# Kernel tuning notes

Measured on AMD Instinct MI355X. Metric: run time of the kernel, lower is better.

## Reference

```python
import jax, jax.numpy as jnp
import numpy as np

B, C, H = 64, 64, 32

def _pm_cross_pairs(ks):
    # Replicates PM_cross(2, ks): pairs (i, i+j) ordered by gap j=1..ks-1, then i.
    a, b = [], []
    for j in range(1, ks):
        for i in range(ks - j):
            a.append(i)
            b.append(i + j)
    return np.array(a, dtype=np.int32), np.array(b, dtype=np.int32)

def setup_inputs() -> dict:
    key = jax.random.key(0)
    k1, k2 = jax.random.split(key)
    ia, ib = _pm_cross_pairs(H)           # 496 pairs for H=32
    hk = ia.shape[0] + 2 * H              # 560
    x = jax.random.normal(k1, (B, C, H, H), dtype=jnp.float32)
    weight = 0.1 * jax.random.normal(k2, (C, H, hk, H), dtype=jnp.float32)
    return {"x": x, "weight": weight, "idx_a": jnp.asarray(ia), "idx_b": jnp.asarray(ib)}

def reference(x, weight, idx_a, idx_b):
    # cross-term products along last axis: [B,C,H,P]
    cross = x[..., idx_a] * x[..., idx_b]
    feat = jnp.concatenate([x, x * x, cross], axis=-1)  # [B,C,H,Hk]
    # per-(channel,row) grouped matmul
    return jnp.einsum('bcij,cijo->bcio', feat, weight)
```

## Files before the change

kernel.cpp:

```cpp
#include <hip/hip_runtime.h>

#define NB 64
#define NC 64
#define NH 32
#define HK 560
#define KPAD 576

typedef __bf16 bf16x8 __attribute__((ext_vector_type(8)));
typedef float f32x4 __attribute__((ext_vector_type(4)));

__global__ __launch_bounds__(256, 4) void hconv_kernel(
    const float* __restrict__ x, const float* __restrict__ w,
    const int* __restrict__ idx_a, const int* __restrict__ idx_b,
    float* __restrict__ out)
{
    __shared__ float s_x[NB][34];
    __shared__ __align__(16) unsigned s_lut[KPAD];
    __shared__ __align__(16) unsigned short s_wT[2][32][72];

    const int t = threadIdx.x;
    const int g = blockIdx.x;
    const int c = g >> 5, i = g & 31;

    {
        const int row = t >> 3;
        const int c4 = (t & 7) * 4;
        const float* xr = x + (((size_t)row * NC + c) * NH + i) * NH;
        const float* xr2 = xr + (size_t)32 * NC * NH * NH;
        float4 v = *(const float4*)(xr + c4);
        float4 v2 = *(const float4*)(xr2 + c4);
        s_x[row][c4] = v.x;  s_x[row][c4 + 1] = v.y;
        s_x[row][c4 + 2] = v.z; s_x[row][c4 + 3] = v.w;
        s_x[row + 32][c4] = v2.x;  s_x[row + 32][c4 + 1] = v2.y;
        s_x[row + 32][c4 + 2] = v2.z; s_x[row + 32][c4 + 3] = v2.w;
        if ((t & 7) == 0) {
            s_x[row][32] = 1.0f;      s_x[row][33] = 0.0f;
            s_x[row + 32][32] = 1.0f; s_x[row + 32][33] = 0.0f;
        }
    }

    for (int k = t; k < KPAD; k += 256) {
        unsigned pa, pb;
        if (k < 32)        { pa = (unsigned)k;        pb = 32u; }
        else if (k < 64)   { pa = (unsigned)(k - 32); pb = pa;  }
        else if (k < HK)   { pa = (unsigned)idx_a[k - 64]; pb = (unsigned)idx_b[k - 64]; }
        else               { pa = 33u; pb = 33u; }
        s_lut[k] = pa | (pb << 16);
    }

    const int wv = t >> 6;
    const int lane = t & 63;
    const int lr = lane & 15;
    const int lq = lane >> 4;
    const int row = wv * 16 + lr;
    const int wo = t & 31;
    const int wkg = t >> 5;

    const float* wbase = w + (size_t)(c * NH + i) * HK * NH;

    float pv[8];
    #pragma unroll
    for (int r = 0; r < 8; ++r)
        pv[r] = wbase[(size_t)(wkg * 8 + r) * NH + wo];
    {
        bf16x8 wv8;
        #pragma unroll
        for (int r = 0; r < 8; ++r) wv8[r] = (__bf16)pv[r];
        *(bf16x8*)&s_wT[0][wo][wkg * 8] = wv8;
    }
    __syncthreads();

    f32x4 acc0 = {0.f, 0.f, 0.f, 0.f};
    f32x4 acc1 = {0.f, 0.f, 0.f, 0.f};

    for (int ch = 0; ch < 9; ++ch) {
        const int k0 = ch * 64;
        const int buf = ch & 1;

        if (ch < 8) {
            const int kb = k0 + 64 + wkg * 8;
            #pragma unroll
            for (int r = 0; r < 8; ++r) {
                const int k = kb + r;
                pv[r] = (k < HK) ? wbase[(size_t)k * NH + wo] : 0.0f;
            }
        }

        #pragma unroll
        for (int ks = 0; ks < 2; ++ks) {
            const uint4* lp = (const uint4*)&s_lut[k0 + ks * 32 + lq * 8];
            const uint4 L0 = lp[0], L1 = lp[1];
            const unsigned pr[8] = {L0.x, L0.y, L0.z, L0.w, L1.x, L1.y, L1.z, L1.w};
            bf16x8 a;
            #pragma unroll
            for (int j = 0; j < 8; ++j) {
                const float p = s_x[row][pr[j] & 0xffffu] * s_x[row][pr[j] >> 16];
                a[j] = (__bf16)p;
            }
            bf16x8 b0 = *(const bf16x8*)&s_wT[buf][lr][ks * 32 + lq * 8];
            bf16x8 b1 = *(const bf16x8*)&s_wT[buf][16 + lr][ks * 32 + lq * 8];
            acc0 = __builtin_amdgcn_mfma_f32_16x16x32_bf16(a, b0, acc0, 0, 0, 0);
            acc1 = __builtin_amdgcn_mfma_f32_16x16x32_bf16(a, b1, acc1, 0, 0, 0);
        }

        if (ch < 8) {
            bf16x8 wv8;
            #pragma unroll
            for (int r = 0; r < 8; ++r) wv8[r] = (__bf16)pv[r];
            *(bf16x8*)&s_wT[buf ^ 1][wo][wkg * 8] = wv8;
        }
        __syncthreads();
    }

    #pragma unroll
    for (int r = 0; r < 4; ++r) {
        const int b = wv * 16 + lq * 4 + r;
        float* op = out + (((size_t)b * NC + c) * NH + i) * NH;
        op[lr] = acc0[r];
        op[16 + lr] = acc1[r];
    }
}

extern "C" void kernel_launch(void* const* d_in, const int* in_sizes, int n_in,
                              void* d_out, int out_size, void* d_ws, size_t ws_size,
                              hipStream_t stream) {
    const float* x = (const float*)d_in[0];
    const float* w = (const float*)d_in[1];
    const int* idx_a = (const int*)d_in[2];
    const int* idx_b = (const int*)d_in[3];
    float* out = (float*)d_out;
    hconv_kernel<<<dim3(NC * NH), dim3(256), 0, stream>>>(x, w, idx_a, idx_b, out);
}
```

Measured before the change: 238.8 us.

## Replace per-element gather LUT with contiguous octet descriptors over padded x rows

Regroups the K dimension into 8-wide octets whose operands are contiguous runs in x (pairs sharing a gap j), so each lane reads two contiguous 8-float spans instead of 16 indexed gathers. Descriptors encode source offsets, weight row offset and valid count, and partial octets are zero-padded, which grows K from 9 to 11 chunks of 64. The index inputs are no longer read; the pair order is hardcoded to match PM_cross. Weight loads also switch to nontemporal.

Measured after the change: 278.6 us. 16.7% more time.

```diff
diff --git a/kernel.cpp b/kernel.cpp
--- a/kernel.cpp
+++ b/kernel.cpp
@@ -4,7 +4,9 @@
 #define NC 64
 #define NH 32
 #define HK 560
-#define KPAD 576
+#define NOCT 88
+#define NCHUNK 11
+#define XSTR 50
 
 typedef __bf16 bf16x8 __attribute__((ext_vector_type(8)));
 typedef float f32x4 __attribute__((ext_vector_type(4)));
@@ -14,8 +16,8 @@
     const int* __restrict__ idx_a, const int* __restrict__ idx_b,
     float* __restrict__ out)
 {
-    __shared__ float s_x[NB][34];
-    __shared__ __align__(16) unsigned s_lut[KPAD];
+    __shared__ float s_x[NB * XSTR];
+    __shared__ unsigned s_desc[NOCT];
     __shared__ __align__(16) unsigned short s_wT[2][32][72];
 
     const int t = threadIdx.x;
@@ -23,49 +25,63 @@
     const int c = g >> 5, i = g & 31;
 
     {
-        const int row = t >> 3;
-        const int c4 = (t & 7) * 4;
-        const float* xr = x + (((size_t)row * NC + c) * NH + i) * NH;
-        const float* xr2 = xr + (size_t)32 * NC * NH * NH;
-        float4 v = *(const float4*)(xr + c4);
-        float4 v2 = *(const float4*)(xr2 + c4);
-        s_x[row][c4] = v.x;  s_x[row][c4 + 1] = v.y;
-        s_x[row][c4 + 2] = v.z; s_x[row][c4 + 3] = v.w;
-        s_x[row + 32][c4] = v2.x;  s_x[row + 32][c4 + 1] = v2.y;
-        s_x[row + 32][c4 + 2] = v2.z; s_x[row + 32][c4 + 3] = v2.w;
-        if ((t & 7) == 0) {
-            s_x[row][32] = 1.0f;      s_x[row][33] = 0.0f;
-            s_x[row + 32][32] = 1.0f; s_x[row + 32][33] = 0.0f;
+        const int xrow = t >> 2, seg = t & 3;
+        const float* xr = x + (((size_t)xrow * NC + c) * NH + i) * NH + seg * 8;
+        float4 v0 = *(const float4*)(xr);
+        float4 v1 = *(const float4*)(xr + 4);
+        float* dst = &s_x[xrow * XSTR + seg * 8];
+        dst[0] = v0.x; dst[1] = v0.y; dst[2] = v0.z; dst[3] = v0.w;
+        dst[4] = v1.x; dst[5] = v1.y; dst[6] = v1.z; dst[7] = v1.w;
+        if (seg == 0) {
+            #pragma unroll
+            for (int m = 0; m < 8; ++m) {
+                s_x[xrow * XSTR + 32 + m] = 0.0f;
+                s_x[xrow * XSTR + 40 + m] = 1.0f;
+            }
         }
     }
 
-    for (int k = t; k < KPAD; k += 256) {
-        unsigned pa, pb;
-        if (k < 32)        { pa = (unsigned)k;        pb = 32u; }
-        else if (k < 64)   { pa = (unsigned)(k - 32); pb = pa;  }
-        else if (k < HK)   { pa = (unsigned)idx_a[k - 64]; pb = (unsigned)idx_b[k - 64]; }
-        else               { pa = 33u; pb = 33u; }
-        s_lut[k] = pa | (pb << 16);
+    if (t < NOCT) {
+        unsigned pa, pb, ko, val;
+        if (t < 4)      { pa = 8u * t; pb = 40u; ko = 8u * t; val = 8u; }
+        else if (t < 8) { unsigned u = t - 4; pa = pb = 8u * u; ko = 32u + 8u * u; val = 8u; }
+        else if (t < 84) {
+            unsigned q = t - 8, j, a;
+            if (q < 28)      { j = 1 + q / 4;        a = q % 4; }
+            else if (q < 52) { j = 8 + (q - 28) / 3; a = (q - 28) % 3; }
+            else if (q < 68) { j = 16 + (q - 52) / 2; a = (q - 52) % 2; }
+            else             { j = 24 + (q - 68);     a = 0; }
+            unsigned r = 32 - j;
+            pa = 8 * a; pb = 8 * a + j;
+            unsigned rem = r - 8 * a;
+            val = rem < 8u ? rem : 8u;
+            ko = 64u + (j - 1) * 32u - (j * (j - 1)) / 2u + 8u * a;
+        } else { pa = 40u; pb = 40u; ko = 0u; val = 0u; }
+        s_desc[t] = pa | (pb << 6) | (ko << 12) | (val << 22);
     }
 
     const int wv = t >> 6;
     const int lane = t & 63;
     const int lr = lane & 15;
     const int lq = lane >> 4;
-    const int row = wv * 16 + lr;
+    const int arow = wv * 16 + lr;
     const int wo = t & 31;
     const int wkg = t >> 5;
 
     const float* wbase = w + (size_t)(c * NH + i) * HK * NH;
 
-    float pv[8];
-    #pragma unroll
-    for (int r = 0; r < 8; ++r)
-        pv[r] = wbase[(size_t)(wkg * 8 + r) * NH + wo];
+    __syncthreads();
+
     {
+        const unsigned d = s_desc[wkg];
+        const unsigned ko = (d >> 12) & 0x3ffu, val = d >> 22;
         bf16x8 wv8;
         #pragma unroll
-        for (int r = 0; r < 8; ++r) wv8[r] = (__bf16)pv[r];
+        for (int r = 0; r < 8; ++r) {
+            float v = (r < (int)val)
+                ? __builtin_nontemporal_load(&wbase[(size_t)(ko + r) * NH + wo]) : 0.0f;
+            wv8[r] = (__bf16)v;
+        }
         *(bf16x8*)&s_wT[0][wo][wkg * 8] = wv8;
     }
     __syncthreads();
@@ -73,37 +89,35 @@
     f32x4 acc0 = {0.f, 0.f, 0.f, 0.f};
     f32x4 acc1 = {0.f, 0.f, 0.f, 0.f};
 
-    for (int ch = 0; ch < 9; ++ch) {
-        const int k0 = ch * 64;
+    for (int ch = 0; ch < NCHUNK; ++ch) {
         const int buf = ch & 1;
 
-        if (ch < 8) {
-            const int kb = k0 + 64 + wkg * 8;
+        float pv[8];
+        if (ch + 1 < NCHUNK) {
+            const unsigned d = s_desc[(ch + 1) * 8 + wkg];
+            const unsigned ko = (d >> 12) & 0x3ffu, val = d >> 22;
             #pragma unroll
-            for (int r = 0; r < 8; ++r) {
-                const int k = kb + r;
-                pv[r] = (k < HK) ? wbase[(size_t)k * NH + wo] : 0.0f;
-            }
+            for (int r = 0; r < 8; ++r)
+                pv[r] = (r < (int)val)
+                    ? __builtin_nontemporal_load(&wbase[(size_t)(ko + r) * NH + wo]) : 0.0f;
         }
 
         #pragma unroll
         for (int ks = 0; ks < 2; ++ks) {
-            const uint4* lp = (const uint4*)&s_lut[k0 + ks * 32 + lq * 8];
-            const uint4 L0 = lp[0], L1 = lp[1];
-            const unsigned pr[8] = {L0.x, L0.y, L0.z, L0.w, L1.x, L1.y, L1.z, L1.w};
+            const unsigned d = s_desc[ch * 8 + ks * 4 + lq];
+            const float* pA = &s_x[arow * XSTR + (d & 63u)];
+            const float* pB = &s_x[arow * XSTR + ((d >> 6) & 63u)];
             bf16x8 a;
             #pragma unroll
-            for (int j = 0; j < 8; ++j) {
-                const float p = s_x[row][pr[j] & 0xffffu] * s_x[row][pr[j] >> 16];
-                a[j] = (__bf16)p;
-            }
+            for (int j2 = 0; j2 < 8; ++j2)
+                a[j2] = (__bf16)(pA[j2] * pB[j2]);
             bf16x8 b0 = *(const bf16x8*)&s_wT[buf][lr][ks * 32 + lq * 8];
             bf16x8 b1 = *(const bf16x8*)&s_wT[buf][16 + lr][ks * 32 + lq * 8];
             acc0 = __builtin_amdgcn_mfma_f32_16x16x32_bf16(a, b0, acc0, 0, 0, 0);
             acc1 = __builtin_amdgcn_mfma_f32_16x16x32_bf16(a, b1, acc1, 0, 0, 0);
         }
 
-        if (ch < 8) {
+        if (ch + 1 < NCHUNK) {
             bf16x8 wv8;
             #pragma unroll
             for (int r = 0; r < 8; ++r) wv8[r] = (__bf16)pv[r];
```
